# Performance work log

Hardware: AMD Instinct MI355X
Metric: run time of the kernel (lower is better)

## Reference

```python
import jax, jax.numpy as jnp
import numpy as np

B, T, D, H = 256, 256, 384, 64  # batch, seq (BLOCK_SIZE), D_MODEL, HEAD_SIZE


def setup_inputs() -> dict:
    key = jax.random.key(0)
    k1, k2, k3, k4 = jax.random.split(key, 4)
    x = jax.random.normal(k1, (B, T, D), dtype=jnp.float32)
    # nn.Linear(D, H, bias=False): weight [H, D]; we store transposed [D, H] for x @ W
    Wq = jax.random.normal(k2, (D, H), dtype=jnp.float32) * (1.0 / np.sqrt(D))
    Wk = jax.random.normal(k3, (D, H), dtype=jnp.float32) * (1.0 / np.sqrt(D))
    Wv = jax.random.normal(k4, (D, H), dtype=jnp.float32) * (1.0 / np.sqrt(D))
    return {"x": x, "Wq": Wq, "Wk": Wk, "Wv": Wv}


def reference(x, Wq, Wk, Wv):
    # x: [B, T, D]
    q = x @ Wq  # [B, T, H]
    k = x @ Wk  # [B, T, H]
    v = x @ Wv  # [B, T, H]
    scale = 1.0 / jnp.sqrt(jnp.asarray(k.shape[-1], dtype=x.dtype))
    wei = jnp.einsum('bth,bsh->bts', q, k) * scale  # [B, T, T]
    causal = jnp.tril(jnp.ones((x.shape[1], x.shape[1]), dtype=bool))
    wei = jnp.where(causal, wei, -jnp.inf)
    wei = jax.nn.softmax(wei, axis=-1)
    # dropout is identity in eval mode (deterministic reference)
    out = jnp.einsum('bts,bsh->bth', wei, v)  # [B, T, H]
    return out
```

## Files before the change

kernel.cpp:

```cpp
#include <hip/hip_runtime.h>

#define BATCH 256
#define TT 256
#define DD 384
#define HH 64
#define SCALE 0.125f
#define SHIFT 14.0f

typedef __attribute__((ext_vector_type(8))) short short8;
typedef __attribute__((ext_vector_type(4))) float floatx4;

#define KS_STRIDE 72
#define QS_STRIDE 72
#define VT_STRIDE 264
#define PS_STRIDE 40

__device__ __forceinline__ unsigned short f2bf(float f) {
    unsigned int u = __float_as_uint(f);
    u += 0x7fffu + ((u >> 16) & 1u);
    return (unsigned short)(u >> 16);
}
__device__ __forceinline__ float bf2f(unsigned short u) {
    return __uint_as_float(((unsigned int)u) << 16);
}

__device__ __forceinline__ void gld_lds16(const float* g, float* ldst) {
    __builtin_amdgcn_global_load_lds(
        (__attribute__((address_space(1))) void*)(unsigned long long)(const void*)g,
        (__attribute__((address_space(3))) void*)(unsigned int)(unsigned long long)(void*)ldst,
        16, 0, 0);
}

__global__ void pack_w_kernel(const float* __restrict__ wq,
                              const float* __restrict__ wk,
                              const float* __restrict__ wv,
                              unsigned short* __restrict__ wf) {
    int idx = blockIdx.x * 256 + threadIdx.x;
    if (idx >= 3 * DD * HH) return;
    int j = idx & 7;
    int lane = (idx >> 3) & 63;
    int nt = (idx >> 9) & 3;
    int rem = idx >> 11;
    int mat = rem % 3;
    int ch = rem / 3;
    int l16 = lane & 15, q = lane >> 4;
    int h = 16 * nt + l16;
    int d = 32 * ch + 8 * q + j;
    const float* w = (mat == 0) ? wq : (mat == 1) ? wk : wv;
    wf[idx] = f2bf(w[d * HH + h]);
}

__device__ __forceinline__ short8 afrag(const float* xsbuf, int row, int quad) {
    int r7 = row & 7;
    float4 f0 = *(const float4*)(xsbuf + row * 32 + ((2 * quad) ^ r7) * 4);
    float4 f1 = *(const float4*)(xsbuf + row * 32 + ((2 * quad + 1) ^ r7) * 4);
    short8 a;
    a[0] = (short)f2bf(f0.x); a[1] = (short)f2bf(f0.y);
    a[2] = (short)f2bf(f0.z); a[3] = (short)f2bf(f0.w);
    a[4] = (short)f2bf(f1.x); a[5] = (short)f2bf(f1.y);
    a[6] = (short)f2bf(f1.z); a[7] = (short)f2bf(f1.w);
    return a;
}

__global__ __launch_bounds__(512, 2)
void fused_kernel(const float* __restrict__ x, const unsigned short* __restrict__ wfrag,
                  float* __restrict__ out) {
    __shared__ __align__(16) unsigned short Ks[TT * KS_STRIDE];
    __shared__ __align__(16) unsigned short Vt[HH * VT_STRIDE];
    __shared__ __align__(16) union StageU {
        float xs[2][TT * 32];
        struct {
            unsigned short q[TT * QS_STRIDE];
            unsigned short p[8][16 * PS_STRIDE];
        } s;
    } U;

    const int b = blockIdx.x;
    const int tid = threadIdx.x;
    const int wave = tid >> 6;
    const int lane = tid & 63;
    const int quad = lane >> 4;
    const int l16 = lane & 15;

    const float* xb = x + (size_t)b * TT * DD;

    floatx4 cq[2][4] = {};
    floatx4 ck[2][4] = {};
    floatx4 cv[2][4] = {};

    #define STAGE_X(buf_, kk_)                                                    \
        {                                                                         \
            _Pragma("unroll")                                                     \
            for (int rr = 0; rr < 4; ++rr) {                                      \
                int u = rr * 512 + wave * 64 + lane;                              \
                int row_ = u >> 3;                                                \
                int slot_ = (u & 7) ^ (row_ & 7);                                 \
                gld_lds16(xb + row_ * DD + (kk_) + slot_ * 4,                     \
                          U.xs[buf_] + (rr * 512 + wave * 64) * 4);               \
            }                                                                     \
        }

    short8 wf[12], wfn[12];
    #pragma unroll
    for (int i = 0; i < 12; ++i)
        wf[i] = *(const short8*)(wfrag + (size_t)i * 512 + lane * 8);
    STAGE_X(0, 0);

    for (int ch = 0; ch < 12; ++ch) {
        __syncthreads();
        if (ch + 1 < 12) {
            #pragma unroll
            for (int i = 0; i < 12; ++i)
                wfn[i] = *(const short8*)(wfrag + (size_t)((ch + 1) * 12 + i) * 512 + lane * 8);
            STAGE_X((ch + 1) & 1, (ch + 1) * 32);
        }
        const float* xsb = U.xs[ch & 1];
        short8 a0 = afrag(xsb, 32 * wave + l16, quad);
        short8 a1 = afrag(xsb, 32 * wave + 16 + l16, quad);
        #pragma unroll
        for (int nt = 0; nt < 4; ++nt) {
            cq[0][nt] = __builtin_amdgcn_mfma_f32_16x16x32_bf16(a0, wf[nt], cq[0][nt], 0, 0, 0);
            cq[1][nt] = __builtin_amdgcn_mfma_f32_16x16x32_bf16(a1, wf[nt], cq[1][nt], 0, 0, 0);
            ck[0][nt] = __builtin_amdgcn_mfma_f32_16x16x32_bf16(a0, wf[4 + nt], ck[0][nt], 0, 0, 0);
            ck[1][nt] = __builtin_amdgcn_mfma_f32_16x16x32_bf16(a1, wf[4 + nt], ck[1][nt], 0, 0, 0);
            cv[0][nt] = __builtin_amdgcn_mfma_f32_16x16x32_bf16(a0, wf[8 + nt], cv[0][nt], 0, 0, 0);
            cv[1][nt] = __builtin_amdgcn_mfma_f32_16x16x32_bf16(a1, wf[8 + nt], cv[1][nt], 0, 0, 0);
        }
        #pragma unroll
        for (int i = 0; i < 12; ++i) wf[i] = wfn[i];
    }

    __syncthreads();

    #pragma unroll
    for (int mi = 0; mi < 2; ++mi)
      #pragma unroll
      for (int nt = 0; nt < 4; ++nt)
        #pragma unroll
        for (int r = 0; r < 4; ++r) {
            int row = 32 * wave + 16 * mi + 4 * quad + r;
            int col = 16 * nt + l16;
            U.s.q[row * QS_STRIDE + col] = f2bf(cq[mi][nt][r]);
            Ks[row * KS_STRIDE + col] = f2bf(ck[mi][nt][r]);
            Vt[col * VT_STRIDE + row] = f2bf(cv[mi][nt][r]);
        }

    __syncthreads();

    floatx4 o[2][4] = {};
    float l_run[2][4] = {{0.f, 0.f, 0.f, 0.f}, {0.f, 0.f, 0.f, 0.f}};
    unsigned short* psw = U.s.p[wave];

    #pragma unroll
    for (int gi = 0; gi < 2; ++gi) {
        int g = gi ? (15 - wave) : wave;
        int gr0 = 16 * g;
        short8 aq0 = *(const short8*)(U.s.q + (gr0 + l16) * QS_STRIDE + quad * 8);
        short8 aq1 = *(const short8*)(U.s.q + (gr0 + l16) * QS_STRIDE + 32 + quad * 8);
        int clast = g >> 1;
        for (int c = 0; c <= clast; ++c) {
            floatx4 s[2] = {};
            #pragma unroll
            for (int ni = 0; ni < 2; ++ni) {
                const unsigned short* kbase =
                    Ks + (size_t)(32 * c + 16 * ni + l16) * KS_STRIDE + quad * 8;
                s[ni] = __builtin_amdgcn_mfma_f32_16x16x32_bf16(aq0, *(const short8*)(kbase), s[ni], 0, 0, 0);
                s[ni] = __builtin_amdgcn_mfma_f32_16x16x32_bf16(aq1, *(const short8*)(kbase + 32), s[ni], 0, 0, 0);
            }
            bool partial = (c == clast);
            #pragma unroll
            for (int r = 0; r < 4; ++r) {
                int row = gr0 + 4 * quad + r;
                float p0 = __expf(s[0][r] * SCALE - SHIFT);
                float p1 = __expf(s[1][r] * SCALE - SHIFT);
                if (partial) {
                    if (32 * c + l16 > row) p0 = 0.f;
                    if (32 * c + 16 + l16 > row) p1 = 0.f;
                }
                unsigned short b0 = f2bf(p0), b1 = f2bf(p1);
                l_run[gi][r] += bf2f(b0) + bf2f(b1);
                psw[(4 * quad + r) * PS_STRIDE + l16] = b0;
                psw[(4 * quad + r) * PS_STRIDE + 16 + l16] = b1;
            }
            short8 ap = *(const short8*)(psw + l16 * PS_STRIDE + quad * 8);
            #pragma unroll
            for (int nt = 0; nt < 4; ++nt) {
                short8 bv = *(const short8*)(Vt + (size_t)(16 * nt + l16) * VT_STRIDE + 32 * c + quad * 8);
                o[gi][nt] = __builtin_amdgcn_mfma_f32_16x16x32_bf16(ap, bv, o[gi][nt], 0, 0, 0);
            }
        }
    }

    float* outb = out + (size_t)b * TT * HH;
    #pragma unroll
    for (int gi = 0; gi < 2; ++gi) {
        int g = gi ? (15 - wave) : wave;
        #pragma unroll
        for (int r = 0; r < 4; ++r) {
            float l = l_run[gi][r];
            l += __shfl_xor(l, 1);
            l += __shfl_xor(l, 2);
            l += __shfl_xor(l, 4);
            l += __shfl_xor(l, 8);
            l_run[gi][r] = l;
        }
        #pragma unroll
        for (int nt = 0; nt < 4; ++nt)
          #pragma unroll
          for (int r = 0; r < 4; ++r) {
            int row = 16 * g + 4 * quad + r;
            outb[(size_t)row * HH + 16 * nt + l16] = o[gi][nt][r] / l_run[gi][r];
          }
    }
}

extern "C" void kernel_launch(void* const* d_in, const int* in_sizes, int n_in,
                              void* d_out, int out_size, void* d_ws, size_t ws_size,
                              hipStream_t stream) {
    const float* x  = (const float*)d_in[0];
    const float* wq = (const float*)d_in[1];
    const float* wk = (const float*)d_in[2];
    const float* wv = (const float*)d_in[3];
    unsigned short* wf = (unsigned short*)d_ws;
    float* o = (float*)d_out;

    pack_w_kernel<<<(3 * DD * HH + 255) / 256, 256, 0, stream>>>(wq, wk, wv, wf);
    fused_kernel<<<BATCH, 512, 0, stream>>>(x, wf, o);
}
```

Baseline: 168.7 us.

## Split fused kernel into QKV projection and attention kernels via MFMA-fragment workspace

Replaces the single per-batch fused kernel with two kernels. The first projects 128-row tiles of x into Q, K and V, writing them to global workspace in bf16 MFMA-fragment order. The second assigns one 16-row query group per wave and reads K and V fragments straight from global/L2. This gives smaller blocks and more of them, for better occupancy and load balance across CUs. The cost is a global round trip for Q/K/V, an extra launch, and K/V fragments re-read per wave instead of shared through LDS.

```diff
diff --git a/kernel.cpp b/kernel.cpp
--- a/kernel.cpp
+++ b/kernel.cpp
@@ -10,10 +10,8 @@
 typedef __attribute__((ext_vector_type(8))) short short8;
 typedef __attribute__((ext_vector_type(4))) float floatx4;
 
-#define KS_STRIDE 72
-#define QS_STRIDE 72
-#define VT_STRIDE 264
 #define PS_STRIDE 40
+#define SC_STRIDE 72
 
 __device__ __forceinline__ unsigned short f2bf(float f) {
     unsigned int u = __float_as_uint(f);
@@ -62,27 +60,19 @@
     return a;
 }
 
-__global__ __launch_bounds__(512, 2)
-void fused_kernel(const float* __restrict__ x, const unsigned short* __restrict__ wfrag,
-                  float* __restrict__ out) {
-    __shared__ __align__(16) unsigned short Ks[TT * KS_STRIDE];
-    __shared__ __align__(16) unsigned short Vt[HH * VT_STRIDE];
-    __shared__ __align__(16) union StageU {
-        float xs[2][TT * 32];
-        struct {
-            unsigned short q[TT * QS_STRIDE];
-            unsigned short p[8][16 * PS_STRIDE];
-        } s;
-    } U;
-
-    const int b = blockIdx.x;
+__global__ __launch_bounds__(256, 3)
+void qkv_kernel(const float* __restrict__ x, const unsigned short* __restrict__ wfrag,
+                unsigned short* __restrict__ qa, unsigned short* __restrict__ kf,
+                unsigned short* __restrict__ vf) {
+    __shared__ __align__(16) float xs[2][128 * 32];
+    __shared__ __align__(16) unsigned short Scratch[4 * 2560];
+
     const int tid = threadIdx.x;
     const int wave = tid >> 6;
     const int lane = tid & 63;
     const int quad = lane >> 4;
     const int l16 = lane & 15;
-
-    const float* xb = x + (size_t)b * TT * DD;
+    const int R0 = blockIdx.x * 128;
 
     floatx4 cq[2][4] = {};
     floatx4 ck[2][4] = {};
@@ -92,11 +82,11 @@
         {                                                                         \
             _Pragma("unroll")                                                     \
             for (int rr = 0; rr < 4; ++rr) {                                      \
-                int u = rr * 512 + wave * 64 + lane;                              \
+                int u = rr * 256 + wave * 64 + lane;                              \
                 int row_ = u >> 3;                                                \
                 int slot_ = (u & 7) ^ (row_ & 7);                                 \
-                gld_lds16(xb + row_ * DD + (kk_) + slot_ * 4,                     \
-                          U.xs[buf_] + (rr * 512 + wave * 64) * 4);               \
+                gld_lds16(x + (size_t)(R0 + row_) * DD + (kk_) + slot_ * 4,       \
+                          xs[buf_] + (rr * 256 + wave * 64) * 4);                 \
             }                                                                     \
         }
 
@@ -114,7 +104,7 @@
                 wfn[i] = *(const short8*)(wfrag + (size_t)((ch + 1) * 12 + i) * 512 + lane * 8);
             STAGE_X((ch + 1) & 1, (ch + 1) * 32);
         }
-        const float* xsb = U.xs[ch & 1];
+        const float* xsb = xs[ch & 1];
         short8 a0 = afrag(xsb, 32 * wave + l16, quad);
         short8 a1 = afrag(xsb, 32 * wave + 16 + l16, quad);
         #pragma unroll
@@ -130,88 +120,138 @@
         for (int i = 0; i < 12; ++i) wf[i] = wfn[i];
     }
 
-    __syncthreads();
+    unsigned short* scr = Scratch + wave * 2560;
 
     #pragma unroll
     for (int mi = 0; mi < 2; ++mi)
       #pragma unroll
       for (int nt = 0; nt < 4; ++nt)
         #pragma unroll
+        for (int r = 0; r < 4; ++r)
+            scr[(16 * mi + 4 * quad + r) * SC_STRIDE + 16 * nt + l16] = f2bf(cq[mi][nt][r]);
+    #pragma unroll
+    for (int mi = 0; mi < 2; ++mi) {
+        int g = blockIdx.x * 8 + wave * 2 + mi;
+        #pragma unroll
+        for (int ks = 0; ks < 2; ++ks) {
+            short8 f = *(const short8*)(scr + (16 * mi + l16) * SC_STRIDE + 32 * ks + quad * 8);
+            *(short8*)(qa + ((size_t)(g * 2 + ks) * 64 + lane) * 8) = f;
+        }
+    }
+
+    #pragma unroll
+    for (int mi = 0; mi < 2; ++mi)
+      #pragma unroll
+      for (int nt = 0; nt < 4; ++nt)
+        #pragma unroll
+        for (int r = 0; r < 4; ++r)
+            scr[(16 * mi + 4 * quad + r) * SC_STRIDE + 16 * nt + l16] = f2bf(ck[mi][nt][r]);
+    #pragma unroll
+    for (int mi = 0; mi < 2; ++mi) {
+        int g = blockIdx.x * 8 + wave * 2 + mi;
+        #pragma unroll
+        for (int ks = 0; ks < 2; ++ks) {
+            short8 f = *(const short8*)(scr + (16 * mi + l16) * SC_STRIDE + 32 * ks + quad * 8);
+            *(short8*)(kf + ((size_t)(g * 2 + ks) * 64 + lane) * 8) = f;
+        }
+    }
+
+    const int C = blockIdx.x * 4 + wave;
+    #pragma unroll
+    for (int hh = 0; hh < 2; ++hh) {
+        #pragma unroll
+        for (int ntl = 0; ntl < 2; ++ntl)
+          #pragma unroll
+          for (int mi = 0; mi < 2; ++mi)
+            #pragma unroll
+            for (int r = 0; r < 4; ++r)
+                scr[(16 * ntl + l16) * SC_STRIDE + 16 * mi + 4 * quad + r] =
+                    f2bf(cv[mi][2 * hh + ntl][r]);
+        #pragma unroll
+        for (int ntl = 0; ntl < 2; ++ntl) {
+            short8 f = *(const short8*)(scr + (16 * ntl + l16) * SC_STRIDE + quad * 8);
+            *(short8*)(vf + ((size_t)(C * 4 + 2 * hh + ntl) * 64 + lane) * 8) = f;
+        }
+    }
+}
+
+__global__ __launch_bounds__(256, 4)
+void attn_kernel(const unsigned short* __restrict__ qa, const unsigned short* __restrict__ kf,
+                 const unsigned short* __restrict__ vf, float* __restrict__ out) {
+    __shared__ __align__(16) unsigned short ps[4][16 * PS_STRIDE];
+
+    const int tid = threadIdx.x;
+    const int wave = tid >> 6;
+    const int lane = tid & 63;
+    const int quad = lane >> 4;
+    const int l16 = lane & 15;
+
+    const int g = blockIdx.x * 4 + wave;
+    const int b = g >> 4;
+    const int gl = g & 15;
+
+    short8 aq[2];
+    #pragma unroll
+    for (int ks = 0; ks < 2; ++ks)
+        aq[ks] = *(const short8*)(qa + ((size_t)(g * 2 + ks) * 64 + lane) * 8);
+
+    floatx4 o[4] = {};
+    float l_run[4] = {0.f, 0.f, 0.f, 0.f};
+    unsigned short* psw = ps[wave];
+    const int cmax = gl >> 1;
+
+    for (int c = 0; c <= cmax; ++c) {
+        floatx4 s[2] = {};
+        #pragma unroll
+        for (int ni = 0; ni < 2; ++ni) {
+            int kg = b * 16 + 2 * c + ni;
+            #pragma unroll
+            for (int ks = 0; ks < 2; ++ks) {
+                short8 bk = *(const short8*)(kf + ((size_t)(kg * 2 + ks) * 64 + lane) * 8);
+                s[ni] = __builtin_amdgcn_mfma_f32_16x16x32_bf16(aq[ks], bk, s[ni], 0, 0, 0);
+            }
+        }
+        bool partial = (c == cmax);
+        #pragma unroll
         for (int r = 0; r < 4; ++r) {
-            int row = 32 * wave + 16 * mi + 4 * quad + r;
-            int col = 16 * nt + l16;
-            U.s.q[row * QS_STRIDE + col] = f2bf(cq[mi][nt][r]);
-            Ks[row * KS_STRIDE + col] = f2bf(ck[mi][nt][r]);
-            Vt[col * VT_STRIDE + row] = f2bf(cv[mi][nt][r]);
-        }
-
-    __syncthreads();
-
-    floatx4 o[2][4] = {};
-    float l_run[2][4] = {{0.f, 0.f, 0.f, 0.f}, {0.f, 0.f, 0.f, 0.f}};
-    unsigned short* psw = U.s.p[wave];
-
-    #pragma unroll
-    for (int gi = 0; gi < 2; ++gi) {
-        int g = gi ? (15 - wave) : wave;
-        int gr0 = 16 * g;
-        short8 aq0 = *(const short8*)(U.s.q + (gr0 + l16) * QS_STRIDE + quad * 8);
-        short8 aq1 = *(const short8*)(U.s.q + (gr0 + l16) * QS_STRIDE + 32 + quad * 8);
-        int clast = g >> 1;
-        for (int c = 0; c <= clast; ++c) {
-            floatx4 s[2] = {};
-            #pragma unroll
-            for (int ni = 0; ni < 2; ++ni) {
-                const unsigned short* kbase =
-                    Ks + (size_t)(32 * c + 16 * ni + l16) * KS_STRIDE + quad * 8;
-                s[ni] = __builtin_amdgcn_mfma_f32_16x16x32_bf16(aq0, *(const short8*)(kbase), s[ni], 0, 0, 0);
-                s[ni] = __builtin_amdgcn_mfma_f32_16x16x32_bf16(aq1, *(const short8*)(kbase + 32), s[ni], 0, 0, 0);
+            int row = 16 * gl + 4 * quad + r;
+            float p0 = __expf(s[0][r] * SCALE - SHIFT);
+            float p1 = __expf(s[1][r] * SCALE - SHIFT);
+            if (partial) {
+                if (32 * c + l16 > row) p0 = 0.f;
+                if (32 * c + 16 + l16 > row) p1 = 0.f;
             }
-            bool partial = (c == clast);
-            #pragma unroll
-            for (int r = 0; r < 4; ++r) {
-                int row = gr0 + 4 * quad + r;
-                float p0 = __expf(s[0][r] * SCALE - SHIFT);
-                float p1 = __expf(s[1][r] * SCALE - SHIFT);
-                if (partial) {
-                    if (32 * c + l16 > row) p0 = 0.f;
-                    if (32 * c + 16 + l16 > row) p1 = 0.f;
-                }
-                unsigned short b0 = f2bf(p0), b1 = f2bf(p1);
-                l_run[gi][r] += bf2f(b0) + bf2f(b1);
-                psw[(4 * quad + r) * PS_STRIDE + l16] = b0;
-                psw[(4 * quad + r) * PS_STRIDE + 16 + l16] = b1;
-            }
-            short8 ap = *(const short8*)(psw + l16 * PS_STRIDE + quad * 8);
-            #pragma unroll
-            for (int nt = 0; nt < 4; ++nt) {
-                short8 bv = *(const short8*)(Vt + (size_t)(16 * nt + l16) * VT_STRIDE + 32 * c + quad * 8);
-                o[gi][nt] = __builtin_amdgcn_mfma_f32_16x16x32_bf16(ap, bv, o[gi][nt], 0, 0, 0);
-            }
-        }
-    }
-
+            unsigned short b0 = f2bf(p0), b1 = f2bf(p1);
+            l_run[r] += bf2f(b0) + bf2f(b1);
+            psw[(4 * quad + r) * PS_STRIDE + l16] = b0;
+            psw[(4 * quad + r) * PS_STRIDE + 16 + l16] = b1;
+        }
+        short8 ap = *(const short8*)(psw + l16 * PS_STRIDE + quad * 8);
+        int C = b * 8 + c;
+        #pragma unroll
+        for (int nt = 0; nt < 4; ++nt) {
+            short8 bv = *(const short8*)(vf + ((size_t)(C * 4 + nt) * 64 + lane) * 8);
+            o[nt] = __builtin_amdgcn_mfma_f32_16x16x32_bf16(ap, bv, o[nt], 0, 0, 0);
+        }
+    }
+
+    #pragma unroll
+    for (int r = 0; r < 4; ++r) {
+        float l = l_run[r];
+        l += __shfl_xor(l, 1);
+        l += __shfl_xor(l, 2);
+        l += __shfl_xor(l, 4);
+        l += __shfl_xor(l, 8);
+        l_run[r] = l;
+    }
     float* outb = out + (size_t)b * TT * HH;
     #pragma unroll
-    for (int gi = 0; gi < 2; ++gi) {
-        int g = gi ? (15 - wave) : wave;
-        #pragma unroll
-        for (int r = 0; r < 4; ++r) {
-            float l = l_run[gi][r];
-            l += __shfl_xor(l, 1);
-            l += __shfl_xor(l, 2);
-            l += __shfl_xor(l, 4);
-            l += __shfl_xor(l, 8);
-            l_run[gi][r] = l;
-        }
-        #pragma unroll
-        for (int nt = 0; nt < 4; ++nt)
-          #pragma unroll
-          for (int r = 0; r < 4; ++r) {
-            int row = 16 * g + 4 * quad + r;
-            outb[(size_t)row * HH + 16 * nt + l16] = o[gi][nt][r] / l_run[gi][r];
-          }
-    }
+    for (int nt = 0; nt < 4; ++nt)
+      #pragma unroll
+      for (int r = 0; r < 4; ++r) {
+        int row = 16 * gl + 4 * quad + r;
+        outb[(size_t)row * HH + 16 * nt + l16] = o[nt][r] / l_run[r];
+      }
 }
 
 extern "C" void kernel_launch(void* const* d_in, const int* in_sizes, int n_in,
@@ -221,9 +261,14 @@
     const float* wq = (const float*)d_in[1];
     const float* wk = (const float*)d_in[2];
     const float* wv = (const float*)d_in[3];
+    float* o = (float*)d_out;
+
     unsigned short* wf = (unsigned short*)d_ws;
-    float* o = (float*)d_out;
+    unsigned short* qa = (unsigned short*)((char*)d_ws + 0x30000);
+    unsigned short* kf = (unsigned short*)((char*)d_ws + 0x30000 + 0x800000);
+    unsigned short* vf = (unsigned short*)((char*)d_ws + 0x30000 + 0x1000000);
 
     pack_w_kernel<<<(3 * DD * HH + 255) / 256, 256, 0, stream>>>(wq, wk, wv, wf);
-    fused_kernel<<<BATCH, 512, 0, stream>>>(x, wf, o);
-}
+    qkv_kernel<<<512, 256, 0, stream>>>(x, wf, qa, kf, vf);
+    attn_kernel<<<1024, 256, 0, stream>>>(qa, kf, vf, o);
+}
```

Measured after the change: 213.2 us. 1.26x slower.
